# Performance work log

Hardware: AMD Instinct MI355X
Metric: run time of the kernel (lower is better)

Reference implementation:

```python
import jax, jax.numpy as jnp
import numpy as np

B, G, CI, H, W, CO = 32, 1, 128, 48, 48, 128

def setup_inputs() -> dict:
    key = jax.random.key(0)
    k1, k2, k3 = jax.random.split(key, 3)
    x = jax.random.normal(k1, (B, G, CI, H, W, 1, 1), dtype=jnp.float32)
    b = jax.random.normal(k2, (B, G, CI, H, W, 1, 1), dtype=jnp.float32)
    weights = jax.random.normal(k3, (CI, G, CO, H, W, 1, 1), dtype=jnp.float32)
    return {"x": x, "b": b, "weights": weights}

def reference(x, b, weights):
    # Locally-connected 1x1 conv: per-(h,w) [i->j] contraction, grouped.
    out_b = jnp.einsum('bgihwkc,igjhwkc->bgjhw', b, weights)  # [B,G,CO,H,W]
    out_x = jnp.einsum('bgihwkc,igjhwkc->bgjhw', x, weights)  # [B,G,CO,H,W]
    # Spatially center the b-path, then add the x-path.
    return out_b - jnp.mean(out_b, axis=(-2, -1), keepdims=True) + out_x
```

## Files before the change

### kernel.cpp

```cpp
#include <hip/hip_runtime.h>

#define HWN 2304
#define HT  4
#define JT  64
#define NTHR 256

using bf16x8 = __attribute__((ext_vector_type(8))) short;
using f32x4  = __attribute__((ext_vector_type(4))) float;

union Lds {
    struct {
        unsigned short sA[128 * 40];
        unsigned short bA[128 * 40];
        unsigned short wB[256 * 40];
    } st;
    float outst[2048 * 4];
};

__device__ __forceinline__ unsigned short f2bf(float x) {
    unsigned u = __float_as_uint(x);
    u += 0x7FFF + ((u >> 16) & 1);
    return (unsigned short)(u >> 16);
}

__global__ __launch_bounds__(NTHR, 4)
void lc_main(const float* __restrict__ xg, const float* __restrict__ bg,
             const float* __restrict__ wg, float* __restrict__ outg,
             float* __restrict__ mg) {
    __shared__ Lds L;

    const int bid  = blockIdx.x;
    const int unit = (bid & 7) * 144 + (bid >> 3);
    const int hc  = unit >> 1;
    const int jh  = unit & 1;
    const int hw0 = hc * HT;
    const int j0  = jh * JT;

    const int t   = threadIdx.x;
    const int wv  = t >> 6;
    const int l   = t & 63;
    const int mw  = wv & 1;
    const int np  = wv >> 1;
    const int l15 = l & 15;
    const int blk = l >> 4;

    const int kq = t & 7;
    const int bb = t >> 3;

    f32x4 accS[2][HT];
    f32x4 accB[2];
    const f32x4 zz = {0.f, 0.f, 0.f, 0.f};
#pragma unroll
    for (int n = 0; n < 2; ++n) {
        accB[n] = zz;
#pragma unroll
        for (int h = 0; h < HT; ++h) accS[n][h] = zz;
    }

    for (int kc = 0; kc < 4; ++kc) {
        f32x4 rx[4], rb[4];
#pragma unroll
        for (int d = 0; d < 4; ++d) {
            const int row = bb * 128 + kc * 32 + kq * 4 + d;
            rx[d] = *(const f32x4*)(xg + row * HWN + hw0);
            rb[d] = *(const f32x4*)(bg + row * HWN + hw0);
        }
        __syncthreads();
#pragma unroll
        for (int h = 0; h < 4; ++h) {
            ushort4 s4 = { f2bf(rx[0][h] + rb[0][h]), f2bf(rx[1][h] + rb[1][h]),
                           f2bf(rx[2][h] + rb[2][h]), f2bf(rx[3][h] + rb[3][h]) };
            ushort4 b4 = { f2bf(rb[0][h]), f2bf(rb[1][h]),
                           f2bf(rb[2][h]), f2bf(rb[3][h]) };
            const int rsb = (h * 32 + bb) * 40 + kq * 4;
            *(ushort4*)&L.st.sA[rsb] = s4;
            *(ushort4*)&L.st.bA[rsb] = b4;
        }
        f32x4 rw[2][4];
#pragma unroll
        for (int jd = 0; jd < 2; ++jd)
#pragma unroll
        for (int d = 0; d < 4; ++d) {
            const int i = kc * 32 + kq * 4 + d;
            rw[jd][d] = *(const f32x4*)(wg + (i * 128 + j0 + bb + jd * 32) * HWN + hw0);
        }
#pragma unroll
        for (int jd = 0; jd < 2; ++jd)
#pragma unroll
        for (int h = 0; h < 4; ++h) {
            ushort4 w4 = { f2bf(rw[jd][0][h]), f2bf(rw[jd][1][h]),
                           f2bf(rw[jd][2][h]), f2bf(rw[jd][3][h]) };
            *(ushort4*)&L.st.wB[(h * 64 + bb + jd * 32) * 40 + kq * 4] = w4;
        }
        __syncthreads();
#pragma unroll
        for (int h = 0; h < 4; ++h) {
            bf16x8 aS = *(const bf16x8*)&L.st.sA[(h * 32 + mw * 16 + l15) * 40 + blk * 8];
            bf16x8 aB = *(const bf16x8*)&L.st.bA[(h * 32 + mw * 16 + l15) * 40 + blk * 8];
#pragma unroll
            for (int n = 0; n < 2; ++n) {
                bf16x8 wf = *(const bf16x8*)&L.st.wB[(h * 64 + (np * 2 + n) * 16 + l15) * 40 + blk * 8];
                accS[n][h] = __builtin_amdgcn_mfma_f32_16x16x32_bf16(aS, wf, accS[n][h], 0, 0, 0);
                accB[n]    = __builtin_amdgcn_mfma_f32_16x16x32_bf16(aB, wf, accB[n],    0, 0, 0);
            }
        }
    }

    __syncthreads();
#pragma unroll
    for (int n = 0; n < 2; ++n) {
        const int jc = (np * 2 + n) * 16 + l15;
#pragma unroll
        for (int r = 0; r < 4; ++r) {
            const int p = (mw * 16 + blk * 4 + r) * 64 + jc;
#pragma unroll
            for (int h = 0; h < 4; ++h)
                L.outst[p * 4 + h] = accS[n][h][r];
        }
    }
    __syncthreads();
#pragma unroll
    for (int i = 0; i < 8; ++i) {
        const int p = i * 256 + t;
        const float4 v = *(const float4*)&L.outst[p * 4];
        const int br = p >> 6, jl = p & 63;
        *(float4*)(outg + (br * 128 + j0 + jl) * HWN + hw0) = v;
    }
#pragma unroll
    for (int n = 0; n < 2; ++n) {
        const int jc = j0 + (np * 2 + n) * 16 + l15;
#pragma unroll
        for (int r = 0; r < 4; ++r)
            atomicAdd(&mg[(mw * 16 + blk * 4 + r) * 128 + jc], accB[n][r]);
    }
}

__global__ __launch_bounds__(576)
void lc_fix(float* __restrict__ outg, const float* __restrict__ mg) {
    const int bj = blockIdx.x;
    const float m = mg[bj] * (1.0f / 2304.0f);
    float4* p = (float4*)(outg + bj * HWN) + threadIdx.x;
    float4 v = *p;
    v.x -= m; v.y -= m; v.z -= m; v.w -= m;
    *p = v;
}

extern "C" void kernel_launch(void* const* d_in, const int* in_sizes, int n_in,
                              void* d_out, int out_size, void* d_ws, size_t ws_size,
                              hipStream_t stream) {
    const float* x = (const float*)d_in[0];
    const float* b = (const float*)d_in[1];
    const float* w = (const float*)d_in[2];
    float* out = (float*)d_out;
    float* m   = (float*)d_ws;

    hipMemsetAsync(m, 0, 32 * 128 * sizeof(float), stream);
    lc_main<<<1152, NTHR, 0, stream>>>(x, b, w, out, m);
    lc_fix<<<4096, 576, 0, stream>>>(out, m);
}
```

Before: 380.7 us.

## Use 512 threads, prefetch next K chunk, and replicate mean accumulators to cut atomic contention

Doubles the threads per block, so each wave owns one 16-column slice of the output and each thread loads a smaller share of the input. It issues the global loads for the next K chunk before the MFMA work on the current chunk, overlapping memory latency with compute. The mean-reduction atomics go to up to 64 replicated copies of the accumulator array, selected by block index, and the fix kernel sums those copies with a wavefront shuffle. In exchange there is a larger memset, more register pressure under launch_bounds(512,4), and an extra reduction step in the fix kernel.

```diff
diff --git a/kernel.cpp b/kernel.cpp
--- a/kernel.cpp
+++ b/kernel.cpp
@@ -3,7 +3,7 @@
 #define HWN 2304
 #define HT  4
 #define JT  64
-#define NTHR 256
+#define NTHR 512
 
 using bf16x8 = __attribute__((ext_vector_type(8))) short;
 using f32x4  = __attribute__((ext_vector_type(4))) float;
@@ -26,7 +26,7 @@
 __global__ __launch_bounds__(NTHR, 4)
 void lc_main(const float* __restrict__ xg, const float* __restrict__ bg,
              const float* __restrict__ wg, float* __restrict__ outg,
-             float* __restrict__ mg) {
+             float* __restrict__ rep, int repmask) {
     __shared__ Lds L;
 
     const int bid  = blockIdx.x;
@@ -40,106 +40,109 @@
     const int wv  = t >> 6;
     const int l   = t & 63;
     const int mw  = wv & 1;
-    const int np  = wv >> 1;
+    const int nq  = wv >> 1;
     const int l15 = l & 15;
     const int blk = l >> 4;
 
-    const int kq = t & 7;
-    const int bb = t >> 3;
+    const int kp = t & 15;
+    const int bb = t >> 4;
+    const int jj = t & 63;
+    const int ii = t >> 6;
 
-    f32x4 accS[2][HT];
-    f32x4 accB[2];
-    const f32x4 zz = {0.f, 0.f, 0.f, 0.f};
+    const float* xbase = xg + hw0;
+    const float* bbase = bg + hw0;
+    const float* wbase = wg + (size_t)(j0 + jj) * HWN + hw0;
+
+    f32x4 rx[2], rb[2], rw[4];
+
+    auto load_chunk = [&](int kc) {
 #pragma unroll
-    for (int n = 0; n < 2; ++n) {
-        accB[n] = zz;
+        for (int d = 0; d < 2; ++d) {
+            const int row = bb * 128 + kc * 32 + kp * 2 + d;
+            rx[d] = *(const f32x4*)(xbase + (size_t)row * HWN);
+            rb[d] = *(const f32x4*)(bbase + (size_t)row * HWN);
+        }
 #pragma unroll
-        for (int h = 0; h < HT; ++h) accS[n][h] = zz;
-    }
+        for (int e = 0; e < 4; ++e) {
+            const int i = kc * 32 + ii * 4 + e;
+            rw[e] = *(const f32x4*)(wbase + (size_t)i * (128 * HWN));
+        }
+    };
 
-    for (int kc = 0; kc < 4; ++kc) {
-        f32x4 rx[4], rb[4];
-#pragma unroll
-        for (int d = 0; d < 4; ++d) {
-            const int row = bb * 128 + kc * 32 + kq * 4 + d;
-            rx[d] = *(const f32x4*)(xg + row * HWN + hw0);
-            rb[d] = *(const f32x4*)(bg + row * HWN + hw0);
-        }
-        __syncthreads();
+    auto stage = [&]() {
 #pragma unroll
         for (int h = 0; h < 4; ++h) {
-            ushort4 s4 = { f2bf(rx[0][h] + rb[0][h]), f2bf(rx[1][h] + rb[1][h]),
-                           f2bf(rx[2][h] + rb[2][h]), f2bf(rx[3][h] + rb[3][h]) };
-            ushort4 b4 = { f2bf(rb[0][h]), f2bf(rb[1][h]),
-                           f2bf(rb[2][h]), f2bf(rb[3][h]) };
-            const int rsb = (h * 32 + bb) * 40 + kq * 4;
-            *(ushort4*)&L.st.sA[rsb] = s4;
-            *(ushort4*)&L.st.bA[rsb] = b4;
-        }
-        f32x4 rw[2][4];
-#pragma unroll
-        for (int jd = 0; jd < 2; ++jd)
-#pragma unroll
-        for (int d = 0; d < 4; ++d) {
-            const int i = kc * 32 + kq * 4 + d;
-            rw[jd][d] = *(const f32x4*)(wg + (i * 128 + j0 + bb + jd * 32) * HWN + hw0);
+            ushort2 s2 = { f2bf(rx[0][h] + rb[0][h]), f2bf(rx[1][h] + rb[1][h]) };
+            ushort2 b2 = { f2bf(rb[0][h]), f2bf(rb[1][h]) };
+            const int off = (h * 32 + bb) * 40 + kp * 2;
+            *(ushort2*)&L.st.sA[off] = s2;
+            *(ushort2*)&L.st.bA[off] = b2;
         }
 #pragma unroll
-        for (int jd = 0; jd < 2; ++jd)
+        for (int h = 0; h < 4; ++h) {
+            ushort4 w4 = { f2bf(rw[0][h]), f2bf(rw[1][h]),
+                           f2bf(rw[2][h]), f2bf(rw[3][h]) };
+            *(ushort4*)&L.st.wB[(h * 64 + jj) * 40 + ii * 4] = w4;
+        }
+    };
+
+    f32x4 accS[4];
+    f32x4 accB = {0.f, 0.f, 0.f, 0.f};
 #pragma unroll
-        for (int h = 0; h < 4; ++h) {
-            ushort4 w4 = { f2bf(rw[jd][0][h]), f2bf(rw[jd][1][h]),
-                           f2bf(rw[jd][2][h]), f2bf(rw[jd][3][h]) };
-            *(ushort4*)&L.st.wB[(h * 64 + bb + jd * 32) * 40 + kq * 4] = w4;
-        }
+    for (int h = 0; h < 4; ++h) accS[h] = {0.f, 0.f, 0.f, 0.f};
+
+    load_chunk(0);
+    for (int kc = 0; kc < 4; ++kc) {
         __syncthreads();
+        stage();
+        __syncthreads();
+        if (kc < 3) load_chunk(kc + 1);
 #pragma unroll
         for (int h = 0; h < 4; ++h) {
             bf16x8 aS = *(const bf16x8*)&L.st.sA[(h * 32 + mw * 16 + l15) * 40 + blk * 8];
             bf16x8 aB = *(const bf16x8*)&L.st.bA[(h * 32 + mw * 16 + l15) * 40 + blk * 8];
-#pragma unroll
-            for (int n = 0; n < 2; ++n) {
-                bf16x8 wf = *(const bf16x8*)&L.st.wB[(h * 64 + (np * 2 + n) * 16 + l15) * 40 + blk * 8];
-                accS[n][h] = __builtin_amdgcn_mfma_f32_16x16x32_bf16(aS, wf, accS[n][h], 0, 0, 0);
-                accB[n]    = __builtin_amdgcn_mfma_f32_16x16x32_bf16(aB, wf, accB[n],    0, 0, 0);
-            }
+            bf16x8 wf = *(const bf16x8*)&L.st.wB[(h * 64 + nq * 16 + l15) * 40 + blk * 8];
+            accS[h] = __builtin_amdgcn_mfma_f32_16x16x32_bf16(aS, wf, accS[h], 0, 0, 0);
+            accB    = __builtin_amdgcn_mfma_f32_16x16x32_bf16(aB, wf, accB,    0, 0, 0);
         }
     }
 
     __syncthreads();
 #pragma unroll
-    for (int n = 0; n < 2; ++n) {
-        const int jc = (np * 2 + n) * 16 + l15;
+    for (int r = 0; r < 4; ++r) {
+        const int p = (mw * 16 + blk * 4 + r) * 64 + nq * 16 + l15;
 #pragma unroll
-        for (int r = 0; r < 4; ++r) {
-            const int p = (mw * 16 + blk * 4 + r) * 64 + jc;
-#pragma unroll
-            for (int h = 0; h < 4; ++h)
-                L.outst[p * 4 + h] = accS[n][h][r];
-        }
+        for (int h = 0; h < 4; ++h)
+            L.outst[p * 4 + h] = accS[h][r];
     }
     __syncthreads();
 #pragma unroll
-    for (int i = 0; i < 8; ++i) {
-        const int p = i * 256 + t;
+    for (int i = 0; i < 4; ++i) {
+        const int p = i * 512 + t;
         const float4 v = *(const float4*)&L.outst[p * 4];
         const int br = p >> 6, jl = p & 63;
-        *(float4*)(outg + (br * 128 + j0 + jl) * HWN + hw0) = v;
+        *(float4*)(outg + (size_t)(br * 128 + j0 + jl) * HWN + hw0) = v;
     }
+    const int rr = bid & repmask;
 #pragma unroll
-    for (int n = 0; n < 2; ++n) {
-        const int jc = j0 + (np * 2 + n) * 16 + l15;
-#pragma unroll
-        for (int r = 0; r < 4; ++r)
-            atomicAdd(&mg[(mw * 16 + blk * 4 + r) * 128 + jc], accB[n][r]);
-    }
+    for (int r = 0; r < 4; ++r)
+        atomicAdd(&rep[rr * 4096 + (mw * 16 + blk * 4 + r) * 128 + j0 + nq * 16 + l15],
+                  accB[r]);
 }
 
 __global__ __launch_bounds__(576)
-void lc_fix(float* __restrict__ outg, const float* __restrict__ mg) {
+void lc_fix(float* __restrict__ outg, const float* __restrict__ rep, int nrep) {
     const int bj = blockIdx.x;
-    const float m = mg[bj] * (1.0f / 2304.0f);
-    float4* p = (float4*)(outg + bj * HWN) + threadIdx.x;
+    __shared__ float sm;
+    if (threadIdx.x < 64) {
+        float v = (threadIdx.x < nrep) ? rep[threadIdx.x * 4096 + bj] : 0.f;
+        v += __shfl_xor(v, 32); v += __shfl_xor(v, 16); v += __shfl_xor(v, 8);
+        v += __shfl_xor(v, 4);  v += __shfl_xor(v, 2);  v += __shfl_xor(v, 1);
+        if (threadIdx.x == 0) sm = v * (1.0f / 2304.0f);
+    }
+    __syncthreads();
+    const float m = sm;
+    float4* p = (float4*)(outg + (size_t)bj * HWN) + threadIdx.x;
     float4 v = *p;
     v.x -= m; v.y -= m; v.z -= m; v.w -= m;
     *p = v;
@@ -152,9 +155,12 @@
     const float* b = (const float*)d_in[1];
     const float* w = (const float*)d_in[2];
     float* out = (float*)d_out;
-    float* m   = (float*)d_ws;
+    float* rep = (float*)d_ws;
 
-    hipMemsetAsync(m, 0, 32 * 128 * sizeof(float), stream);
-    lc_main<<<1152, NTHR, 0, stream>>>(x, b, w, out, m);
-    lc_fix<<<4096, 576, 0, stream>>>(out, m);
+    int nrep = 1;
+    while (nrep < 64 && (size_t)(nrep * 2) * 4096 * sizeof(float) <= ws_size) nrep <<= 1;
+
+    hipMemsetAsync(rep, 0, (size_t)nrep * 4096 * sizeof(float), stream);
+    lc_main<<<1152, NTHR, 0, stream>>>(x, b, w, out, rep, nrep - 1);
+    lc_fix<<<4096, 576, 0, stream>>>(out, rep, nrep);
 }
```

Result: no change. 386.3 us (+1.5%).
